# Performance work log

Measured on AMD Instinct MI355X. Metric: run time of the kernel, lower is better.

The kernel has to match this reference:

```python
import jax, jax.numpy as jnp
import numpy as np

TOP_K = 32
TEMPERATURE = 1.0
PARAM_SCALE = 0.02


def setup_inputs() -> dict:
    key = jax.random.key(0)
    ks = jax.random.split(key, 7)
    B, S, D, F, P, R = 2, 1024, 1024, 4096, 256, 64
    x = jax.random.normal(ks[0], (B, S, D), dtype=jnp.float32)
    fc1_A = jax.random.normal(ks[1], (P, D, R), dtype=jnp.float32) * PARAM_SCALE
    fc1_B = jax.random.normal(ks[2], (P, R, F), dtype=jnp.float32) * PARAM_SCALE
    fc2_A = jax.random.normal(ks[3], (P, F, R), dtype=jnp.float32) * PARAM_SCALE
    fc2_B = jax.random.normal(ks[4], (P, R, D), dtype=jnp.float32) * PARAM_SCALE
    fc1_logits = jax.random.normal(ks[5], (P,), dtype=jnp.float32)
    fc2_logits = jax.random.normal(ks[6], (P,), dtype=jnp.float32)
    return {"x": x, "fc1_A": fc1_A, "fc1_B": fc1_B, "fc2_A": fc2_A,
            "fc2_B": fc2_B, "fc1_logits": fc1_logits, "fc2_logits": fc2_logits}


def _compose_weight(logits, A, B):
    """Top-k select primitives, softmax composition weights, weighted low-rank sum.

    A: (P, d_in, r), B: (P, r, d_out) -> W: (d_in, d_out)
    """
    vals, idx = jax.lax.top_k(logits, TOP_K)          # (K,), (K,)
    w = jax.nn.softmax(vals / TEMPERATURE)            # composition weights over selected
    A_sel = A[idx]                                    # (K, d_in, r) gather
    B_sel = B[idx]                                    # (K, r, d_out) gather
    return jnp.einsum('k,kir,kro->io', w, A_sel, B_sel)


def reference(x, fc1_A, fc1_B, fc2_A, fc2_B, fc1_logits, fc2_logits):
    W1 = _compose_weight(fc1_logits, fc1_A, fc1_B)    # (D, F)
    W2 = _compose_weight(fc2_logits, fc2_A, fc2_B)    # (F, D)
    h = jax.nn.gelu(jnp.einsum('bsd,df->bsf', x, W1))
    return jnp.einsum('bsf,fd->bsd', h, W2)
```

## Files before the change

### kernel.cpp

```cpp
#include <hip/hip_runtime.h>
#include <cstdint>
#include <cstddef>

typedef __attribute__((ext_vector_type(8))) short bhalf8;
typedef __attribute__((ext_vector_type(4))) float f32x4;

__device__ __forceinline__ unsigned short f2bf(float f){
    unsigned int u = __float_as_uint(f);
    u += 0x7fffu + ((u >> 16) & 1u);
    return (unsigned short)(u >> 16);
}

__device__ __forceinline__ float gelu_tanh(float x){
    const float c0 = 0.7978845608028654f;
    float x3 = x * x * x;
    float t = tanhf(c0 * (x + 0.044715f * x3));
    return 0.5f * x * (1.0f + t);
}

__device__ __forceinline__ void async_lds16(const unsigned short* g, unsigned short* l){
    __builtin_amdgcn_global_load_lds(
        (const __attribute__((address_space(1))) void*)g,
        (__attribute__((address_space(3))) void*)l, 16, 0, 0);
}

__global__ void topk_softmax_kernel(const float* __restrict__ lg1,
                                    const float* __restrict__ lg2,
                                    int* __restrict__ idx_out,
                                    float* __restrict__ w_out)
{
    const float* lg = (blockIdx.x == 0) ? lg1 : lg2;
    int*   idxo = idx_out + blockIdx.x * 32;
    float* wo   = w_out   + blockIdx.x * 32;
    const int lane = threadIdx.x;
    float v[4];
    #pragma unroll
    for (int j = 0; j < 4; ++j) v[j] = lg[lane * 4 + j];
    __shared__ float svals[32];
    for (int k = 0; k < 32; ++k){
        float bv = -1e30f; int bi = 0;
        #pragma unroll
        for (int j = 0; j < 4; ++j){
            if (v[j] > bv){ bv = v[j]; bi = lane * 4 + j; }
        }
        for (int off = 32; off > 0; off >>= 1){
            float ov = __shfl_down(bv, off);
            int   oi = __shfl_down(bi, off);
            if (ov > bv){ bv = ov; bi = oi; }
        }
        bv = __shfl(bv, 0);
        bi = __shfl(bi, 0);
        if (lane == 0){ svals[k] = bv; idxo[k] = bi; }
        if ((bi >> 2) == lane) v[bi & 3] = -1e30f;
    }
    if (lane == 0){
        float mx = svals[0];
        float sum = 0.f;
        for (int k = 0; k < 32; ++k){ float e = expf(svals[k] - mx); wo[k] = e; sum += e; }
        float inv = 1.f / sum;
        for (int k = 0; k < 32; ++k) wo[k] *= inv;
    }
}

__global__ void convert_bf16_kernel(const float* __restrict__ src,
                                    unsigned short* __restrict__ dst, int n4)
{
    int v = blockIdx.x * 256 + threadIdx.x;
    if (v >= n4) return;
    float4 x = ((const float4*)src)[v];
    ushort4 o; o.x = f2bf(x.x); o.y = f2bf(x.y); o.z = f2bf(x.z); o.w = f2bf(x.w);
    ((ushort4*)dst)[v] = o;
}

__global__ void zero_kernel(float4* __restrict__ p, int n4)
{
    int v = blockIdx.x * 256 + threadIdx.x;
    if (v < n4){ float4 z = {0.f,0.f,0.f,0.f}; p[v] = z; }
}

__global__ void gather_nat_kernel(const float* __restrict__ src,
                                  unsigned short* __restrict__ dst,
                                  const int* __restrict__ idx,
                                  const float* __restrict__ w,
                                  int Drows, int use_scale, int n4)
{
    int v = blockIdx.x * 256 + threadIdx.x;
    if (v >= n4) return;
    int c4 = v & 511;
    int d  = v >> 9;
    int k  = c4 >> 4;
    int r4 = c4 & 15;
    int p  = idx[k];
    float sc = use_scale ? w[k] : 1.0f;
    const float4* s = (const float4*)(src + ((size_t)p * Drows + d) * 64) + r4;
    float4 x = *s;
    ushort4 o;
    o.x = f2bf(sc * x.x); o.y = f2bf(sc * x.y);
    o.z = f2bf(sc * x.z); o.w = f2bf(sc * x.w);
    *(ushort4*)(dst + (size_t)d * 2048 + k * 64 + r4 * 4) = o;
}

__global__ void gather_tr_kernel(const float* __restrict__ src,
                                 unsigned short* __restrict__ dst,
                                 const int* __restrict__ idx,
                                 const float* __restrict__ w,
                                 int Fcols, int use_scale)
{
    const int k  = blockIdx.y;
    const int f0 = blockIdx.x * 64;
    const int p  = idx[k];
    const float sc = use_scale ? w[k] : 1.0f;
    __shared__ float tile[64][65];
    const int t  = threadIdx.x;
    const int cf = t & 15;
    const int r0 = t >> 4;
    #pragma unroll
    for (int pass = 0; pass < 4; ++pass){
        int r = r0 + pass * 16;
        float4 x = *((const float4*)(src + ((size_t)p * 64 + r) * Fcols + f0) + cf);
        tile[r][cf * 4 + 0] = x.x; tile[r][cf * 4 + 1] = x.y;
        tile[r][cf * 4 + 2] = x.z; tile[r][cf * 4 + 3] = x.w;
    }
    __syncthreads();
    const int r4  = t & 15;
    const int fl0 = t >> 4;
    #pragma unroll
    for (int pass = 0; pass < 4; ++pass){
        int fl = fl0 + pass * 16;
        ushort4 o;
        o.x = f2bf(sc * tile[r4 * 4 + 0][fl]);
        o.y = f2bf(sc * tile[r4 * 4 + 1][fl]);
        o.z = f2bf(sc * tile[r4 * 4 + 2][fl]);
        o.w = f2bf(sc * tile[r4 * 4 + 3][fl]);
        *(ushort4*)(dst + (size_t)(f0 + fl) * 2048 + k * 64 + r4 * 4) = o;
    }
}

template<int EPI>
__launch_bounds__(256, 2)
__global__ void gemm_nt_kernel(const unsigned short* __restrict__ A,
                               const unsigned short* __restrict__ Bt,
                               void* __restrict__ Cout,
                               int M, int N, int K, int Kslice)
{
    __shared__ unsigned short sA[128 * 32];
    __shared__ unsigned short sB[128 * 32];
    const int bm = blockIdx.y * 128;
    const int bn = blockIdx.x * 128;
    const int t    = threadIdx.x;
    const int wave = t >> 6;
    const int lane = t & 63;
    const int wr   = (wave >> 1) * 64;
    const int wc   = (wave & 1) * 64;
    const int m16  = lane & 15;
    const int quad = lane >> 4;
    const int srow = t >> 2;
    const int scol = t & 3;

    f32x4 acc[4][4];
    const f32x4 z = {0.f, 0.f, 0.f, 0.f};
    #pragma unroll
    for (int i = 0; i < 4; ++i)
        #pragma unroll
        for (int j = 0; j < 4; ++j) acc[i][j] = z;

    const int kbeg = blockIdx.z * Kslice;
    const unsigned short* Arow = A  + (size_t)(bm + srow) * K + scol * 8 + kbeg;
    const unsigned short* Brow = Bt + (size_t)(bn + srow) * K + scol * 8 + kbeg;
    unsigned short* lA = sA + srow * 32 + scol * 8;
    unsigned short* lB = sB + srow * 32 + scol * 8;

    for (int k0 = 0; k0 < Kslice; k0 += 32){
        async_lds16(Arow + k0,                    lA);
        async_lds16(Arow + (size_t)64 * K + k0,   lA + 64 * 32);
        async_lds16(Brow + k0,                    lB);
        async_lds16(Brow + (size_t)64 * K + k0,   lB + 64 * 32);
        __syncthreads();

        bhalf8 af[4], bfr[4];
        #pragma unroll
        for (int i = 0; i < 4; ++i)
            af[i] = *(const bhalf8*)(sA + (wr + i * 16 + m16) * 32 + quad * 8);
        #pragma unroll
        for (int j = 0; j < 4; ++j)
            bfr[j] = *(const bhalf8*)(sB + (wc + j * 16 + m16) * 32 + quad * 8);

        #pragma unroll
        for (int i = 0; i < 4; ++i)
            #pragma unroll
            for (int j = 0; j < 4; ++j)
                acc[i][j] = __builtin_amdgcn_mfma_f32_16x16x32_bf16(af[i], bfr[j], acc[i][j], 0, 0, 0);
        __syncthreads();
    }

    #pragma unroll
    for (int i = 0; i < 4; ++i){
        #pragma unroll
        for (int j = 0; j < 4; ++j){
            #pragma unroll
            for (int r = 0; r < 4; ++r){
                int row = bm + wr + i * 16 + quad * 4 + r;
                int col = bn + wc + j * 16 + m16;
                float vv = acc[i][j][r];
                if (EPI == 1) vv = gelu_tanh(vv);
                if (EPI == 2)      ((float*)Cout)[(size_t)row * N + col] = vv;
                else if (EPI == 3) atomicAdd(&((float*)Cout)[(size_t)row * N + col], vv);
                else ((unsigned short*)Cout)[(size_t)row * N + col] = f2bf(vv);
            }
        }
    }
}

extern "C" void kernel_launch(void* const* d_in, const int* in_sizes, int n_in,
                              void* d_out, int out_size, void* d_ws, size_t ws_size,
                              hipStream_t stream)
{
    const float* x    = (const float*)d_in[0];
    const float* fc1A = (const float*)d_in[1];
    const float* fc1B = (const float*)d_in[2];
    const float* fc2A = (const float*)d_in[3];
    const float* fc2B = (const float*)d_in[4];
    const float* lg1  = (const float*)d_in[5];
    const float* lg2  = (const float*)d_in[6];
    float* out = (float*)d_out;

    char* ws = (char*)d_ws;
    int*            idxb = (int*)(ws + 0);
    float*          wb   = (float*)(ws + 256);
    unsigned short* x16  = (unsigned short*)(ws + 4096);
    unsigned short* Ag1  = (unsigned short*)(ws + 4096 + (4u << 20));
    unsigned short* Bt1  = (unsigned short*)(ws + 4096 + (8u << 20));
    unsigned short* W1t  = (unsigned short*)(ws + 4096 + (24u << 20));
    unsigned short* hbuf = (unsigned short*)(ws + 4096 + (32u << 20));
    unsigned short* Ag2  = Bt1;
    unsigned short* Bg2t = Ag1;
    unsigned short* W2t  = W1t;

    zero_kernel<<<dim3(2048), dim3(256), 0, stream>>>((float4*)out, 524288);

    topk_softmax_kernel<<<dim3(2), dim3(64), 0, stream>>>(lg1, lg2, idxb, wb);

    convert_bf16_kernel<<<dim3(2048), dim3(256), 0, stream>>>(x, x16, 524288);

    gather_nat_kernel<<<dim3(2048), dim3(256), 0, stream>>>(fc1A, Ag1, idxb, wb, 1024, 1, 524288);
    gather_tr_kernel<<<dim3(64, 32), dim3(256), 0, stream>>>(fc1B, Bt1, idxb, wb, 4096, 0);

    gemm_nt_kernel<0><<<dim3(8, 32), dim3(256), 0, stream>>>(Bt1, Ag1, W1t, 4096, 1024, 2048, 2048);

    gemm_nt_kernel<1><<<dim3(32, 16), dim3(256), 0, stream>>>(x16, W1t, hbuf, 2048, 4096, 1024, 1024);

    gather_nat_kernel<<<dim3(8192), dim3(256), 0, stream>>>(fc2A, Ag2, idxb + 32, wb + 32, 4096, 0, 2097152);
    gather_tr_kernel<<<dim3(16, 32), dim3(256), 0, stream>>>(fc2B, Bg2t, idxb + 32, wb + 32, 1024, 1);

    gemm_nt_kernel<0><<<dim3(32, 8), dim3(256), 0, stream>>>(Bg2t, Ag2, W2t, 1024, 4096, 2048, 2048);

    gemm_nt_kernel<3><<<dim3(8, 16, 4), dim3(256), 0, stream>>>(hbuf, W2t, out, 2048, 1024, 4096, 1024);
}
```

Baseline: 664.7 us.

## Merge weight-compose GEMMs into one launch, fuse prep kernels, double K step

Fuses the bf16 conversion of x and the zeroing of the output into a single prep kernel. The two weight-composition GEMMs (W1 and W2) now run in one launch of 512 blocks, which requires separate workspace buffers instead of aliased ones. The GEMM main loop now loads 64 K elements per barrier pair instead of 32, halving the number of syncs but doubling LDS use per block (32 KB). The aim is to cut launch count and barrier overhead and to give the small compose GEMMs more parallelism, at the cost of more LDS and registers, which may lower occupancy.

Measured after the change: 614.5 us. 7.5% less time.

```diff
diff --git a/kernel.cpp b/kernel.cpp
--- a/kernel.cpp
+++ b/kernel.cpp
@@ -62,20 +62,21 @@
     }
 }
 
-__global__ void convert_bf16_kernel(const float* __restrict__ src,
-                                    unsigned short* __restrict__ dst, int n4)
-{
-    int v = blockIdx.x * 256 + threadIdx.x;
-    if (v >= n4) return;
-    float4 x = ((const float4*)src)[v];
-    ushort4 o; o.x = f2bf(x.x); o.y = f2bf(x.y); o.z = f2bf(x.z); o.w = f2bf(x.w);
-    ((ushort4*)dst)[v] = o;
-}
-
-__global__ void zero_kernel(float4* __restrict__ p, int n4)
-{
-    int v = blockIdx.x * 256 + threadIdx.x;
-    if (v < n4){ float4 z = {0.f,0.f,0.f,0.f}; p[v] = z; }
+__global__ void prep_kernel(const float* __restrict__ src,
+                            unsigned short* __restrict__ dst,
+                            float4* __restrict__ outz)
+{
+    int b = blockIdx.x;
+    if (b < 2048){
+        int v = b * 256 + threadIdx.x;
+        float4 x = ((const float4*)src)[v];
+        ushort4 o; o.x = f2bf(x.x); o.y = f2bf(x.y); o.z = f2bf(x.z); o.w = f2bf(x.w);
+        ((ushort4*)dst)[v] = o;
+    } else {
+        int v = (b - 2048) * 256 + threadIdx.x;
+        float4 z = {0.f,0.f,0.f,0.f};
+        outz[v] = z;
+    }
 }
 
 __global__ void gather_nat_kernel(const float* __restrict__ src,
@@ -137,16 +138,17 @@
 }
 
 template<int EPI>
-__launch_bounds__(256, 2)
-__global__ void gemm_nt_kernel(const unsigned short* __restrict__ A,
-                               const unsigned short* __restrict__ Bt,
-                               void* __restrict__ Cout,
-                               int M, int N, int K, int Kslice)
-{
-    __shared__ unsigned short sA[128 * 32];
-    __shared__ unsigned short sB[128 * 32];
-    const int bm = blockIdx.y * 128;
-    const int bn = blockIdx.x * 128;
+__device__ __forceinline__ void gemm_body(unsigned short* smem,
+                                          const unsigned short* __restrict__ A,
+                                          const unsigned short* __restrict__ Bt,
+                                          void* __restrict__ Cout,
+                                          int N, int K, int Kslice, int kbeg,
+                                          int bm, int bn)
+{
+    unsigned short* sA0 = smem;
+    unsigned short* sA1 = smem + 4096;
+    unsigned short* sB0 = smem + 8192;
+    unsigned short* sB1 = smem + 12288;
     const int t    = threadIdx.x;
     const int wave = t >> 6;
     const int lane = t & 63;
@@ -164,32 +166,47 @@
         #pragma unroll
         for (int j = 0; j < 4; ++j) acc[i][j] = z;
 
-    const int kbeg = blockIdx.z * Kslice;
     const unsigned short* Arow = A  + (size_t)(bm + srow) * K + scol * 8 + kbeg;
     const unsigned short* Brow = Bt + (size_t)(bn + srow) * K + scol * 8 + kbeg;
-    unsigned short* lA = sA + srow * 32 + scol * 8;
-    unsigned short* lB = sB + srow * 32 + scol * 8;
-
-    for (int k0 = 0; k0 < Kslice; k0 += 32){
-        async_lds16(Arow + k0,                    lA);
-        async_lds16(Arow + (size_t)64 * K + k0,   lA + 64 * 32);
-        async_lds16(Brow + k0,                    lB);
-        async_lds16(Brow + (size_t)64 * K + k0,   lB + 64 * 32);
+    const size_t rstep = (size_t)64 * K;
+    unsigned short* lA0 = sA0 + t * 8;
+    unsigned short* lA1 = sA1 + t * 8;
+    unsigned short* lB0 = sB0 + t * 8;
+    unsigned short* lB1 = sB1 + t * 8;
+
+    for (int k0 = 0; k0 < Kslice; k0 += 64){
+        async_lds16(Arow + k0,              lA0);
+        async_lds16(Arow + rstep + k0,      lA0 + 64 * 32);
+        async_lds16(Arow + k0 + 32,         lA1);
+        async_lds16(Arow + rstep + k0 + 32, lA1 + 64 * 32);
+        async_lds16(Brow + k0,              lB0);
+        async_lds16(Brow + rstep + k0,      lB0 + 64 * 32);
+        async_lds16(Brow + k0 + 32,         lB1);
+        async_lds16(Brow + rstep + k0 + 32, lB1 + 64 * 32);
         __syncthreads();
 
-        bhalf8 af[4], bfr[4];
-        #pragma unroll
-        for (int i = 0; i < 4; ++i)
-            af[i] = *(const bhalf8*)(sA + (wr + i * 16 + m16) * 32 + quad * 8);
-        #pragma unroll
-        for (int j = 0; j < 4; ++j)
-            bfr[j] = *(const bhalf8*)(sB + (wc + j * 16 + m16) * 32 + quad * 8);
+        bhalf8 af0[4], bf0[4], af1[4], bf1[4];
+        #pragma unroll
+        for (int i = 0; i < 4; ++i){
+            af0[i] = *(const bhalf8*)(sA0 + (wr + i * 16 + m16) * 32 + quad * 8);
+            af1[i] = *(const bhalf8*)(sA1 + (wr + i * 16 + m16) * 32 + quad * 8);
+        }
+        #pragma unroll
+        for (int j = 0; j < 4; ++j){
+            bf0[j] = *(const bhalf8*)(sB0 + (wc + j * 16 + m16) * 32 + quad * 8);
+            bf1[j] = *(const bhalf8*)(sB1 + (wc + j * 16 + m16) * 32 + quad * 8);
+        }
 
         #pragma unroll
         for (int i = 0; i < 4; ++i)
             #pragma unroll
             for (int j = 0; j < 4; ++j)
-                acc[i][j] = __builtin_amdgcn_mfma_f32_16x16x32_bf16(af[i], bfr[j], acc[i][j], 0, 0, 0);
+                acc[i][j] = __builtin_amdgcn_mfma_f32_16x16x32_bf16(af0[i], bf0[j], acc[i][j], 0, 0, 0);
+        #pragma unroll
+        for (int i = 0; i < 4; ++i)
+            #pragma unroll
+            for (int j = 0; j < 4; ++j)
+                acc[i][j] = __builtin_amdgcn_mfma_f32_16x16x32_bf16(af1[i], bf1[j], acc[i][j], 0, 0, 0);
         __syncthreads();
     }
 
@@ -203,12 +220,43 @@
                 int col = bn + wc + j * 16 + m16;
                 float vv = acc[i][j][r];
                 if (EPI == 1) vv = gelu_tanh(vv);
-                if (EPI == 2)      ((float*)Cout)[(size_t)row * N + col] = vv;
-                else if (EPI == 3) atomicAdd(&((float*)Cout)[(size_t)row * N + col], vv);
+                if (EPI == 3) atomicAdd(&((float*)Cout)[(size_t)row * N + col], vv);
                 else ((unsigned short*)Cout)[(size_t)row * N + col] = f2bf(vv);
             }
         }
     }
+}
+
+__launch_bounds__(256, 2)
+__global__ void gemm13_kernel(const unsigned short* __restrict__ A1,
+                              const unsigned short* __restrict__ B1,
+                              unsigned short* __restrict__ C1,
+                              const unsigned short* __restrict__ A2,
+                              const unsigned short* __restrict__ B2,
+                              unsigned short* __restrict__ C2)
+{
+    __shared__ unsigned short smem[4 * 128 * 32];
+    int id = blockIdx.x;
+    if (id < 256){
+        gemm_body<0>(smem, A1, B1, C1, 1024, 2048, 2048, 0,
+                     (id >> 3) * 128, (id & 7) * 128);
+    } else {
+        id -= 256;
+        gemm_body<0>(smem, A2, B2, C2, 4096, 2048, 2048, 0,
+                     (id >> 5) * 128, (id & 31) * 128);
+    }
+}
+
+template<int EPI>
+__launch_bounds__(256, 2)
+__global__ void gemm_nt_kernel(const unsigned short* __restrict__ A,
+                               const unsigned short* __restrict__ Bt,
+                               void* __restrict__ Cout,
+                               int N, int K, int Kslice)
+{
+    __shared__ unsigned short smem[4 * 128 * 32];
+    gemm_body<EPI>(smem, A, Bt, Cout, N, K, Kslice, blockIdx.z * Kslice,
+                   blockIdx.y * 128, blockIdx.x * 128);
 }
 
 extern "C" void kernel_launch(void* const* d_in, const int* in_sizes, int n_in,
@@ -227,32 +275,28 @@
     char* ws = (char*)d_ws;
     int*            idxb = (int*)(ws + 0);
     float*          wb   = (float*)(ws + 256);
-    unsigned short* x16  = (unsigned short*)(ws + 4096);
-    unsigned short* Ag1  = (unsigned short*)(ws + 4096 + (4u << 20));
-    unsigned short* Bt1  = (unsigned short*)(ws + 4096 + (8u << 20));
-    unsigned short* W1t  = (unsigned short*)(ws + 4096 + (24u << 20));
-    unsigned short* hbuf = (unsigned short*)(ws + 4096 + (32u << 20));
-    unsigned short* Ag2  = Bt1;
-    unsigned short* Bg2t = Ag1;
-    unsigned short* W2t  = W1t;
-
-    zero_kernel<<<dim3(2048), dim3(256), 0, stream>>>((float4*)out, 524288);
+    char* base = ws + 4096;
+    unsigned short* x16  = (unsigned short*)(base);
+    unsigned short* Ag1  = (unsigned short*)(base + (4ull  << 20));
+    unsigned short* Bt1  = (unsigned short*)(base + (8ull  << 20));
+    unsigned short* Ag2  = (unsigned short*)(base + (24ull << 20));
+    unsigned short* Bg2t = (unsigned short*)(base + (40ull << 20));
+    unsigned short* W1t  = (unsigned short*)(base + (44ull << 20));
+    unsigned short* W2t  = (unsigned short*)(base + (52ull << 20));
+    unsigned short* hbuf = (unsigned short*)(base + (60ull << 20));
 
     topk_softmax_kernel<<<dim3(2), dim3(64), 0, stream>>>(lg1, lg2, idxb, wb);
 
-    convert_bf16_kernel<<<dim3(2048), dim3(256), 0, stream>>>(x, x16, 524288);
+    prep_kernel<<<dim3(4096), dim3(256), 0, stream>>>(x, x16, (float4*)out);
 
     gather_nat_kernel<<<dim3(2048), dim3(256), 0, stream>>>(fc1A, Ag1, idxb, wb, 1024, 1, 524288);
     gather_tr_kernel<<<dim3(64, 32), dim3(256), 0, stream>>>(fc1B, Bt1, idxb, wb, 4096, 0);
-
-    gemm_nt_kernel<0><<<dim3(8, 32), dim3(256), 0, stream>>>(Bt1, Ag1, W1t, 4096, 1024, 2048, 2048);
-
-    gemm_nt_kernel<1><<<dim3(32, 16), dim3(256), 0, stream>>>(x16, W1t, hbuf, 2048, 4096, 1024, 1024);
-
     gather_nat_kernel<<<dim3(8192), dim3(256), 0, stream>>>(fc2A, Ag2, idxb + 32, wb + 32, 4096, 0, 2097152);
     gather_tr_kernel<<<dim3(16, 32), dim3(256), 0, stream>>>(fc2B, Bg2t, idxb + 32, wb + 32, 1024, 1);
 
-    gemm_nt_kernel<0><<<dim3(32, 8), dim3(256), 0, stream>>>(Bg2t, Ag2, W2t, 1024, 4096, 2048, 2048);
-
-    gemm_nt_kernel<3><<<dim3(8, 16, 4), dim3(256), 0, stream>>>(hbuf, W2t, out, 2048, 1024, 4096, 1024);
-}
+    gemm13_kernel<<<dim3(512), dim3(256), 0, stream>>>(Bt1, Ag1, W1t, Bg2t, Ag2, W2t);
+
+    gemm_nt_kernel<1><<<dim3(32, 16), dim3(256), 0, stream>>>(x16, W1t, hbuf, 4096, 1024, 1024);
+
+    gemm_nt_kernel<3><<<dim3(8, 16, 4), dim3(256), 0, stream>>>(hbuf, W2t, out, 1024, 4096, 1024);
+}
```
